# Kernel tuning notes

Hardware: AMD Instinct MI355X
Metric: run time of the kernel (lower is better)

Reference implementation:

```python
import jax, jax.numpy as jnp
from jax import lax
import numpy as np

# --- module hyperparams (match S2_GaussianBlur(nr=2048, nc=2048, kernelSize=10, scale=2, RealData=False)) ---
NR, NC, KS, SCALE = 2048, 2048, 10, 2
MTF = np.array([0.38, 0.34, 0.34, 0.26, 0.22, 0.23])  # mtf[[4,5,6,8,10,11]] for scale==2
C = len(MTF)


def _gaussian_kernels():
    # sigmas = scale * sqrt(-2 ln(mtf) / pi^2)
    sigmas = SCALE * np.sqrt(-2.0 * np.log(MTF) / np.pi ** 2)  # (C,)
    end = int(KS / 2) - 0.5
    coords = np.arange(-end, end + 1.0, 1.0)  # (KS,) = [-4.5, ..., 4.5]
    g1 = np.exp(-coords[None, :] ** 2 / (2.0 * sigmas[:, None] ** 2)) / (
        sigmas[:, None] * np.sqrt(2.0 * np.pi))  # (C,KS)
    k = g1[:, :, None] * g1[:, None, :]  # separable outer product -> (C,KS,KS)
    k = k / k.sum(axis=(1, 2), keepdims=True)
    return k.astype(np.float32)


_KERNELS = jnp.asarray(_gaussian_kernels())  # (C,KS,KS), fixed buffers (requires_grad=False)

# Offsets replicating: circular pad by (nr//2, nc//2), conv with full-image kernel B
# (Gaussian patch placed at [row_start:row_end, col_start:col_end], then flipped both
# axes), crop [0:-1, 0:-1].  This collapses exactly to a circular cross-correlation
# with the flipped KSxKS patch at a fixed shift:
_MIDL, _MIDC = NR // 2, NC // 2
_EB = -int(SCALE / 2)
_ROW_START = int(_MIDL - KS / 2 + _EB)
_COL_START = int(_MIDC - KS / 2 + _EB)
_PAD_T = _MIDL + _ROW_START + KS - NR  # left/top circular pad (=4 here)
_PAD_L = _MIDC + _COL_START + KS - NC
assert 0 <= _PAD_T < KS and 0 <= _PAD_L < KS


def setup_inputs() -> dict:
    key = jax.random.key(0)
    x = jax.random.normal(key, (1, C, NR, NC), dtype=jnp.float32)
    return {"x": x}


def _blur(x):
    # circular (wrap) pad so every output pixel sees its KSxKS circular neighborhood
    xpad = jnp.pad(x, ((0, 0), (0, 0), (_PAD_T, KS - 1 - _PAD_T), (_PAD_L, KS - 1 - _PAD_L)), mode="wrap")
    # flipped Gaussian patch (the full-image kernel B was flipped on both axes)
    w = _KERNELS[:, ::-1, ::-1][:, None, :, :]  # (C,1,KS,KS), depthwise
    return lax.conv_general_dilated(
        xpad, w, window_strides=(1, 1), padding="VALID",
        dimension_numbers=("NCHW", "OIHW", "NCHW"), feature_group_count=C)


def reference(x):
    return _blur(x)  # (1,C,NR,NC)
```

## Files before the change

### kernel.cpp

```cpp
#include <hip/hip_runtime.h>
#include <math.h>

constexpr int C  = 6;
constexpr int NR = 2048;
constexpr int NC = 2048;
constexpr int KS = 10;
constexpr int PAD = 4;

constexpr int TX = 64;
constexpr int TY = 64;
constexpr int HT_H = TY + KS - 1;

__device__ __constant__ float MTFf[C] = {0.38f, 0.34f, 0.34f, 0.26f, 0.22f, 0.23f};

__global__ __launch_bounds__(256)
void s2_gaussian_blur_kernel(const float* __restrict__ x, float* __restrict__ out)
{
    __shared__ float Ht[HT_H * TX];

    const int tid = threadIdx.x;
    const int c   = blockIdx.z;
    const int i0  = blockIdx.y * TY;
    const int j0  = blockIdx.x * TX;

    const float* xc = x   + (size_t)c * NR * NC;
    float*       oc = out + (size_t)c * NR * NC;

    float w[KS];
    {
        float mtf    = MTFf[c];
        float sig    = 2.0f * sqrtf(-2.0f * logf(mtf) / (float)(M_PI * M_PI));
        float inv2s2 = 1.0f / (2.0f * sig * sig);
        float s = 0.0f;
        #pragma unroll
        for (int d = 0; d < KS; ++d) {
            float cd = -4.5f + (float)d;
            w[d] = expf(-cd * cd * inv2s2);
            s += w[d];
        }
        #pragma unroll
        for (int d = 0; d < KS; ++d) w[d] /= s;
    }

    const bool interior = (blockIdx.x >= 1) && (blockIdx.x <= (NC / TX) - 2);

    for (int item = tid; item < HT_H * (TX / 8); item += 256) {
        const int r = item >> 3;
        const int g = item & 7;
        const int gr = (i0 + r - PAD + NR) & (NR - 1);
        const float* row = xc + (size_t)gr * NC;

        float v[17];
        if (interior) {
            const float4* p = (const float4*)(row + j0 + 8 * g - PAD);
            float4 a = p[0], b = p[1], d2 = p[2], d3 = p[3];
            v[0]=a.x;  v[1]=a.y;  v[2]=a.z;  v[3]=a.w;
            v[4]=b.x;  v[5]=b.y;  v[6]=b.z;  v[7]=b.w;
            v[8]=d2.x; v[9]=d2.y; v[10]=d2.z; v[11]=d2.w;
            v[12]=d3.x; v[13]=d3.y; v[14]=d3.z; v[15]=d3.w;
            v[16] = row[j0 + 8 * g + 12];
        } else {
            #pragma unroll
            for (int k = 0; k < 17; ++k)
                v[k] = row[(j0 + 8 * g + k - PAD + NC) & (NC - 1)];
        }

        float acc[8];
        #pragma unroll
        for (int o = 0; o < 8; ++o) {
            float a = 0.0f;
            #pragma unroll
            for (int d = 0; d < KS; ++d) a = fmaf(w[d], v[o + d], a);
            acc[o] = a;
        }
        float4* q = (float4*)&Ht[r * TX + 8 * g];
        q[0] = make_float4(acc[0], acc[1], acc[2], acc[3]);
        q[1] = make_float4(acc[4], acc[5], acc[6], acc[7]);
    }

    __syncthreads();

    {
        const int cg = tid & 15;
        const int rg = tid >> 4;
        float acc[4][4] = {{0.f}};

        #pragma unroll
        for (int k = 0; k < 13; ++k) {
            float4 h = *(const float4*)&Ht[(rg * 4 + k) * TX + cg * 4];
            #pragma unroll
            for (int o = 0; o < 4; ++o) {
                const int d = k - o;
                if (d >= 0 && d < KS) {
                    acc[o][0] = fmaf(w[d], h.x, acc[o][0]);
                    acc[o][1] = fmaf(w[d], h.y, acc[o][1]);
                    acc[o][2] = fmaf(w[d], h.z, acc[o][2]);
                    acc[o][3] = fmaf(w[d], h.w, acc[o][3]);
                }
            }
        }

        #pragma unroll
        for (int o = 0; o < 4; ++o) {
            float4* q = (float4*)&oc[(size_t)(i0 + rg * 4 + o) * NC + (j0 + cg * 4)];
            *q = make_float4(acc[o][0], acc[o][1], acc[o][2], acc[o][3]);
        }
    }
}

extern "C" void kernel_launch(void* const* d_in, const int* in_sizes, int n_in,
                              void* d_out, int out_size, void* d_ws, size_t ws_size,
                              hipStream_t stream) {
    const float* x = (const float*)d_in[0];
    float* out = (float*)d_out;
    dim3 grid(NC / TX, NR / TY, C);
    dim3 block(256);
    s2_gaussian_blur_kernel<<<grid, block, 0, stream>>>(x, out);
}
```

Measured before the change: 218.7 us.

## Stream rows through registers for vertical blur instead of shared-memory tiles

Replaces the 2D tiled kernel, which staged horizontal blur results in shared memory, with a row-streaming kernel. Each 256-thread block covers a full image row width (8 columns per thread) over a 16-row strip. The vertical pass accumulates into a rotating set of register accumulators, with the next row's load prefetched. This removes shared memory and the block barrier, but strip halo overhead rises (25 rows read per 16 output rows, versus 73 per 64 before), register pressure is high (about 80 accumulators), and the grid is smaller.

```diff
diff --git a/kernel.cpp b/kernel.cpp
--- a/kernel.cpp
+++ b/kernel.cpp
@@ -1,27 +1,24 @@
 #include <hip/hip_runtime.h>
 #include <math.h>
 
-constexpr int C  = 6;
-constexpr int NR = 2048;
-constexpr int NC = 2048;
-constexpr int KS = 10;
+constexpr int C   = 6;
+constexpr int NR  = 2048;
+constexpr int NC  = 2048;
+constexpr int KS  = 10;
 constexpr int PAD = 4;
 
-constexpr int TX = 64;
-constexpr int TY = 64;
-constexpr int HT_H = TY + KS - 1;
+constexpr int CPT   = 8;
+constexpr int R     = 16;
+constexpr int NITER = R + KS - 1;
 
 __device__ __constant__ float MTFf[C] = {0.38f, 0.34f, 0.34f, 0.26f, 0.22f, 0.23f};
 
-__global__ __launch_bounds__(256)
-void s2_gaussian_blur_kernel(const float* __restrict__ x, float* __restrict__ out)
+__global__ __launch_bounds__(256, 3)
+void s2_blur_stream(const float* __restrict__ x, float* __restrict__ out)
 {
-    __shared__ float Ht[HT_H * TX];
-
-    const int tid = threadIdx.x;
-    const int c   = blockIdx.z;
-    const int i0  = blockIdx.y * TY;
-    const int j0  = blockIdx.x * TX;
+    const int t  = threadIdx.x;
+    const int c  = blockIdx.y;
+    const int r0 = blockIdx.x * R;
 
     const float* xc = x   + (size_t)c * NR * NC;
     float*       oc = out + (size_t)c * NR * NC;
@@ -42,69 +39,73 @@
         for (int d = 0; d < KS; ++d) w[d] /= s;
     }
 
-    const bool interior = (blockIdx.x >= 1) && (blockIdx.x <= (NC / TX) - 2);
+    const int  cb   = t * CPT - PAD;
+    const bool edge = (t == 0) || (t == 255);
 
-    for (int item = tid; item < HT_H * (TX / 8); item += 256) {
-        const int r = item >> 3;
-        const int g = item & 7;
-        const int gr = (i0 + r - PAD + NR) & (NR - 1);
+    float acc[10][CPT];
+    #pragma unroll
+    for (int s = 0; s < 10; ++s)
+        #pragma unroll
+        for (int q = 0; q < CPT; ++q) acc[s][q] = 0.0f;
+
+    auto load_row = [&](int k, float v[17]) {
+        const int gr = (r0 - PAD + k) & (NR - 1);
         const float* row = xc + (size_t)gr * NC;
-
-        float v[17];
-        if (interior) {
-            const float4* p = (const float4*)(row + j0 + 8 * g - PAD);
+        if (!edge) {
+            const float4* p = (const float4*)(row + cb);
             float4 a = p[0], b = p[1], d2 = p[2], d3 = p[3];
-            v[0]=a.x;  v[1]=a.y;  v[2]=a.z;  v[3]=a.w;
-            v[4]=b.x;  v[5]=b.y;  v[6]=b.z;  v[7]=b.w;
-            v[8]=d2.x; v[9]=d2.y; v[10]=d2.z; v[11]=d2.w;
+            v[0]=a.x;   v[1]=a.y;   v[2]=a.z;   v[3]=a.w;
+            v[4]=b.x;   v[5]=b.y;   v[6]=b.z;   v[7]=b.w;
+            v[8]=d2.x;  v[9]=d2.y;  v[10]=d2.z; v[11]=d2.w;
             v[12]=d3.x; v[13]=d3.y; v[14]=d3.z; v[15]=d3.w;
-            v[16] = row[j0 + 8 * g + 12];
+            v[16] = row[cb + 16];
         } else {
             #pragma unroll
-            for (int k = 0; k < 17; ++k)
-                v[k] = row[(j0 + 8 * g + k - PAD + NC) & (NC - 1)];
+            for (int q = 0; q < 17; ++q)
+                v[q] = row[(cb + q) & (NC - 1)];
+        }
+    };
+
+    float vc[17];
+    load_row(0, vc);
+
+    #pragma unroll
+    for (int k = 0; k < NITER; ++k) {
+        float vn[17];
+        if (k + 1 < NITER) load_row(k + 1, vn);
+
+        float H[CPT];
+        #pragma unroll
+        for (int o = 0; o < CPT; ++o) {
+            float a = 0.0f;
+            #pragma unroll
+            for (int d = 0; d < KS; ++d) a = fmaf(w[d], vc[o + d], a);
+            H[o] = a;
         }
 
-        float acc[8];
         #pragma unroll
-        for (int o = 0; o < 8; ++o) {
-            float a = 0.0f;
-            #pragma unroll
-            for (int d = 0; d < KS; ++d) a = fmaf(w[d], v[o + d], a);
-            acc[o] = a;
-        }
-        float4* q = (float4*)&Ht[r * TX + 8 * g];
-        q[0] = make_float4(acc[0], acc[1], acc[2], acc[3]);
-        q[1] = make_float4(acc[4], acc[5], acc[6], acc[7]);
-    }
-
-    __syncthreads();
-
-    {
-        const int cg = tid & 15;
-        const int rg = tid >> 4;
-        float acc[4][4] = {{0.f}};
-
-        #pragma unroll
-        for (int k = 0; k < 13; ++k) {
-            float4 h = *(const float4*)&Ht[(rg * 4 + k) * TX + cg * 4];
-            #pragma unroll
-            for (int o = 0; o < 4; ++o) {
-                const int d = k - o;
-                if (d >= 0 && d < KS) {
-                    acc[o][0] = fmaf(w[d], h.x, acc[o][0]);
-                    acc[o][1] = fmaf(w[d], h.y, acc[o][1]);
-                    acc[o][2] = fmaf(w[d], h.z, acc[o][2]);
-                    acc[o][3] = fmaf(w[d], h.w, acc[o][3]);
-                }
+        for (int o = 0; o < 10; ++o) {
+            const int j = k + o - 9;
+            if (j >= 0 && j < R) {
+                const int   s  = (k + o) % 10;
+                const float wd = w[9 - o];
+                #pragma unroll
+                for (int q = 0; q < CPT; ++q)
+                    acc[s][q] = fmaf(wd, H[q], acc[s][q]);
             }
         }
 
+        if (k >= KS - 1) {
+            const int s = k % 10;
+            float* orow = oc + (size_t)(r0 + k - 9) * NC + t * CPT;
+            ((float4*)orow)[0] = make_float4(acc[s][0], acc[s][1], acc[s][2], acc[s][3]);
+            ((float4*)orow)[1] = make_float4(acc[s][4], acc[s][5], acc[s][6], acc[s][7]);
+            #pragma unroll
+            for (int q = 0; q < CPT; ++q) acc[s][q] = 0.0f;
+        }
+
         #pragma unroll
-        for (int o = 0; o < 4; ++o) {
-            float4* q = (float4*)&oc[(size_t)(i0 + rg * 4 + o) * NC + (j0 + cg * 4)];
-            *q = make_float4(acc[o][0], acc[o][1], acc[o][2], acc[o][3]);
-        }
+        for (int q = 0; q < 17; ++q) vc[q] = vn[q];
     }
 }
 
@@ -113,7 +114,7 @@
                               hipStream_t stream) {
     const float* x = (const float*)d_in[0];
     float* out = (float*)d_out;
-    dim3 grid(NC / TX, NR / TY, C);
+    dim3 grid(NR / R, C);
     dim3 block(256);
-    s2_gaussian_blur_kernel<<<grid, block, 0, stream>>>(x, out);
+    s2_blur_stream<<<grid, block, 0, stream>>>(x, out);
 }
```

New measurement: 445.6 us. +103.7%, slower.
